# Performance work log

Measured on AMD Instinct MI355X. Metric: run time of the kernel, lower is better.

## Reference

```python
import jax, jax.numpy as jnp
import numpy as np

B, T, C, H = 4, 2048, 768, 12
D = C // H  # head dim = 64
EPS = 1e-5


def setup_inputs() -> dict:
    key = jax.random.key(0)
    ks = jax.random.split(key, 12)
    s = lambda fan_in: 1.0 / np.sqrt(fan_in)
    return {
        "x": jax.random.normal(ks[0], (B, T, C), dtype=jnp.float32),
        "ln1_g": jnp.ones((C,), jnp.float32),
        "ln1_b": jnp.zeros((C,), jnp.float32),
        "w_attn": jax.random.normal(ks[1], (C, 3 * C), jnp.float32) * s(C),
        "b_attn": jnp.zeros((3 * C,), jnp.float32),
        "w_aproj": jax.random.normal(ks[2], (C, C), jnp.float32) * s(C),
        "b_aproj": jnp.zeros((C,), jnp.float32),
        "ln2_g": jnp.ones((C,), jnp.float32),
        "ln2_b": jnp.zeros((C,), jnp.float32),
        "w_fc": jax.random.normal(ks[3], (C, 4 * C), jnp.float32) * s(C),
        "b_fc": jnp.zeros((4 * C,), jnp.float32),
        "w_mproj": jax.random.normal(ks[4], (4 * C, C), jnp.float32) * s(4 * C),
        "b_mproj": jnp.zeros((C,), jnp.float32),
    }


def _layernorm(x, g, b):
    mu = jnp.mean(x, axis=-1, keepdims=True)
    var = jnp.mean(jnp.square(x - mu), axis=-1, keepdims=True)
    return (x - mu) * jax.lax.rsqrt(var + EPS) * g + b


def _attention(h, w_attn, b_attn, w_aproj, b_aproj):
    qkv = h @ w_attn + b_attn                          # [B,T,3C]
    q, k, v = jnp.split(qkv, 3, axis=-1)
    q = q.reshape(B, T, H, D)
    k = k.reshape(B, T, H, D)
    v = v.reshape(B, T, H, D)
    att = jnp.einsum("bqhd,bkhd->bhqk", q, k) * (1.0 / np.sqrt(D))
    causal = jnp.tril(jnp.ones((T, T), bool))
    att = jnp.where(causal, att, -jnp.inf)
    att = jax.nn.softmax(att, axis=-1)
    y = jnp.einsum("bhqk,bkhd->bqhd", att, v).reshape(B, T, C)
    return y @ w_aproj + b_aproj


def reference(x, ln1_g, ln1_b, w_attn, b_attn, w_aproj, b_aproj,
              ln2_g, ln2_b, w_fc, b_fc, w_mproj, b_mproj):
    x = x + _attention(_layernorm(x, ln1_g, ln1_b), w_attn, b_attn, w_aproj, b_aproj)
    h = _layernorm(x, ln2_g, ln2_b)
    h = jax.nn.gelu(h @ w_fc + b_fc, approximate=True)  # tanh approximation, matches F.gelu(approximate='tanh')
    x = x + (h @ w_mproj + b_mproj)
    return x
```

## Files before the change

kernel.cpp:

```cpp
#include <hip/hip_runtime.h>


typedef unsigned short ushortT;
typedef unsigned int uintT;
typedef __attribute__((ext_vector_type(8))) __bf16 bf16x8;
typedef __attribute__((ext_vector_type(4))) float f32x4;

#define MFMA16(a, b, c) __builtin_amdgcn_mfma_f32_16x16x32_bf16(a, b, c, 0, 0, 0)

__device__ inline float b2f(ushortT u) {
  return __uint_as_float(((uintT)u) << 16);
}
__device__ inline ushortT f2b(float f) {
  uintT x = __float_as_uint(f);
  uintT r = x + 0x7fffu + ((x >> 16) & 1u);
  return (ushortT)(r >> 16);
}
__device__ inline uintT pack_bf2(float a, float b) {
  return __builtin_amdgcn_perm(__float_as_uint(b), __float_as_uint(a),
                               0x07060302u);
}

__device__ inline float fast_exp2(float x) {
#if __has_builtin(__builtin_amdgcn_exp2f)
  return __builtin_amdgcn_exp2f(x);
#else
  return exp2f(x);
#endif
}

__device__ inline float gelu_tanh(float v) {
  float t = 0.7978845608028654f * (v + 0.044715f * v * v * v);
  return v / (1.0f + __expf(-2.0f * t));
}

__device__ __forceinline__ void glds16(const ushortT* g, ushortT* l) {
  __builtin_amdgcn_global_load_lds(
      (const __attribute__((address_space(1))) unsigned int*)(const void*)g,
      (__attribute__((address_space(3))) unsigned int*)(void*)l, 16, 0, 0);
}

__global__ __launch_bounds__(256) void detect_dtype(
    const ushortT* __restrict__ w, int* __restrict__ flag) {
  __shared__ int red;
  if (threadIdx.x == 0) red = 0;
  __syncthreads();
  int crazy = 0;
  for (int i = threadIdx.x; i < 4096; i += 256) {
    uintT e = (w[2 * i] >> 7) & 0xFF;
    if (e >= 150) crazy = 1;
  }
  if (crazy) atomicOr(&red, 1);
  __syncthreads();
  if (threadIdx.x == 0) *flag = red;
}

struct VecArgs {
  const void* src[8];
  int n[8];
  int dstoff[8];
};
__global__ __launch_bounds__(256) void convert_vecs(
    VecArgs a, ushortT* __restrict__ pv, const int* __restrict__ flag) {
  int fl = *flag;
  int t = blockIdx.y;
  int i = blockIdx.x * 256 + threadIdx.x;
  if (i >= a.n[t]) return;
  float v = fl ? ((const float*)a.src[t])[i] : b2f(((const ushortT*)a.src[t])[i]);
  pv[a.dstoff[t] + i] = f2b(v);
}

__global__ __launch_bounds__(256) void transpose_any(
    const void* __restrict__ in, ushortT* __restrict__ out, int K, int N,
    const int* __restrict__ flag) {
  __shared__ ushortT t[32][33];
  int fl = *flag;
  int n0 = blockIdx.x * 32, k0 = blockIdx.y * 32;
  int x = threadIdx.x, y0 = threadIdx.y;
#pragma unroll
  for (int i = y0; i < 32; i += 8) {
    size_t idx = (size_t)(k0 + i) * N + n0 + x;
    t[i][x] = fl ? f2b(((const float*)in)[idx]) : ((const ushortT*)in)[idx];
  }
  __syncthreads();
#pragma unroll
  for (int i = y0; i < 32; i += 8)
    out[(size_t)(n0 + i) * K + k0 + x] = t[x][i];
}

__global__ __launch_bounds__(256) void vtrans_kernel(
    const ushortT* __restrict__ qkv, ushortT* __restrict__ vt) {
  const int T = 2048, C3 = 2304;
  __shared__ ushortT tile[64][65];
  int bh = blockIdx.y;
  int b = bh / 12, h = bh % 12;
  int t0 = blockIdx.x * 64;
  int col = threadIdx.x & 63, rowi = threadIdx.x >> 6;
#pragma unroll
  for (int rr = rowi; rr < 64; rr += 4)
    tile[rr][col] =
        qkv[((size_t)(b * T + t0 + rr)) * C3 + 1536 + h * 64 + col];
  __syncthreads();
#pragma unroll
  for (int dd = rowi; dd < 64; dd += 4)
    vt[((size_t)bh * 64 + dd) * T + t0 + col] = tile[col][dd];
}

template <int MODE>
__global__ __launch_bounds__(256) void ln_kernel(
    const void* __restrict__ xin, const ushortT* __restrict__ g,
    const ushortT* __restrict__ bb, ushortT* __restrict__ out,
    const int* __restrict__ flag) {
  const int C = 768;
  bool f32;
  if constexpr (MODE == 1) f32 = true; else f32 = (*flag != 0);
  size_t base = (size_t)blockIdx.x * C;
  int tid = threadIdx.x;
  const float* xf = (const float*)xin;
  const ushortT* xb = (const ushortT*)xin;
  float v0 = f32 ? xf[base + tid]       : b2f(xb[base + tid]);
  float v1 = f32 ? xf[base + tid + 256] : b2f(xb[base + tid + 256]);
  float v2 = f32 ? xf[base + tid + 512] : b2f(xb[base + tid + 512]);
  float s = v0 + v1 + v2;
  float q = v0 * v0 + v1 * v1 + v2 * v2;
#pragma unroll
  for (int off = 32; off; off >>= 1) {
    s += __shfl_xor(s, off);
    q += __shfl_xor(q, off);
  }
  __shared__ float as_[4], aq_[4];
  if ((tid & 63) == 0) { as_[tid >> 6] = s; aq_[tid >> 6] = q; }
  __syncthreads();
  s = as_[0] + as_[1] + as_[2] + as_[3];
  q = aq_[0] + aq_[1] + aq_[2] + aq_[3];
  float mu = s * (1.0f / 768.0f);
  float var = q * (1.0f / 768.0f) - mu * mu;
  float rs = rsqrtf(var + 1e-5f);
  ushortT* orow = out + base;
  orow[tid]       = f2b((v0 - mu) * rs * b2f(g[tid])       + b2f(bb[tid]));
  orow[tid + 256] = f2b((v1 - mu) * rs * b2f(g[tid + 256]) + b2f(bb[tid + 256]));
  orow[tid + 512] = f2b((v2 - mu) * rs * b2f(g[tid + 512]) + b2f(bb[tid + 512]));
}

template <int EPI, int BN>
__global__ __launch_bounds__(256, 2) void gemm_8p(
    const ushortT* __restrict__ A, const ushortT* __restrict__ Bt,
    const ushortT* __restrict__ bias, const void* __restrict__ res,
    void* __restrict__ out, int N, int K, int lda, int nbm, int nbn,
    const int* __restrict__ flag) {
  constexpr int MI = (BN == 256) ? 8 : 4;
  constexpr int NI = 4;
  __shared__ ushortT As3[3][128 * 32];
  __shared__ ushortT Bs3[3][BN * 32];
  int fl = (EPI == 2) ? *flag : 0;
  int tid = threadIdx.x;
  int lane = tid & 63, wave = tid >> 6;
  int quad = lane >> 4, n = lane & 15;
  int wm, wn;
  if constexpr (BN == 256) { wm = 0; wn = wave * 64; }
  else { wm = (wave >> 1) * 64; wn = (wave & 1) * 64; }
  int l = blockIdx.x;
  int xcd = l & 7, j = l >> 3;
  int per = (nbm >> 3) * nbn;
  int js = j % per, sp = j / per;
  int m0 = (xcd * (nbm >> 3) + js / nbn) * 128;
  int n0 = (js % nbn) * BN;
  int koff = sp * K;

  int trow = tid >> 2;
  int tc = (((tid & 3) ^ ((trow >> 1) & 3)) << 3);
  const ushortT* ga = A + (size_t)(m0 + trow) * lda + koff + tc;
  const ushortT* gb = Bt + (size_t)(n0 + trow) * lda + koff + tc;

  const int cs = (quad ^ ((n >> 1) & 3)) << 3;

  int kt = K >> 5;
  f32x4 acc[MI][NI] = {};

  auto stage = [&](int tt, int slot) {
    int k0 = tt << 5;
    ushortT* la = &As3[slot][0] + wave * 512;
    ushortT* lb = &Bs3[slot][0] + wave * 512;
    glds16(ga + k0, la);
    glds16(ga + (size_t)64 * lda + k0, la + 2048);
    glds16(gb + k0, lb);
    glds16(gb + (size_t)64 * lda + k0, lb + 2048);
    if constexpr (BN == 256) {
      glds16(gb + (size_t)128 * lda + k0, lb + 4096);
      glds16(gb + (size_t)192 * lda + k0, lb + 6144);
    }
  };

  stage(0, 0);
  stage(1, 1);
  if constexpr (BN == 256)
    asm volatile("s_waitcnt vmcnt(6)" ::: "memory");
  else
    asm volatile("s_waitcnt vmcnt(4)" ::: "memory");
  __builtin_amdgcn_s_barrier();

  int cur = 0;
  for (int t = 0; t < kt; ++t) {
    const ushortT* ca = &As3[cur][0];
    const ushortT* cb = &Bs3[cur][0];
    int nxt = cur + 2; if (nxt >= 3) nxt -= 3;
    bool pf = (t + 2) < kt;
    int pk0 = (t + 2) << 5;
    ushortT* la = &As3[nxt][0] + wave * 512;
    ushortT* lb = &Bs3[nxt][0] + wave * 512;

    bf16x8 af[4], bfr[NI];
#pragma unroll
    for (int i = 0; i < 4; ++i)
      af[i] = *(const bf16x8*)(ca + (wm + i * 16 + n) * 32 + cs);
#pragma unroll
    for (int i = 0; i < NI; ++i)
      bfr[i] = *(const bf16x8*)(cb + (wn + i * 16 + n) * 32 + cs);
    if (pf) {
      glds16(ga + pk0, la);
      glds16(ga + (size_t)64 * lda + pk0, la + 2048);
      glds16(gb + pk0, lb);
      if constexpr (BN == 128)
        glds16(gb + (size_t)64 * lda + pk0, lb + 2048);
    }
    __builtin_amdgcn_s_barrier();
    __builtin_amdgcn_s_setprio(1);
#pragma unroll
    for (int mi = 0; mi < 4; ++mi)
#pragma unroll
      for (int ni = 0; ni < NI; ++ni)
        acc[mi][ni] = MFMA16(af[mi], bfr[ni], acc[mi][ni]);
    __builtin_amdgcn_s_setprio(0);
    if constexpr (BN == 256) {
      __builtin_amdgcn_s_barrier();
#pragma unroll
      for (int i = 0; i < 4; ++i)
        af[i] = *(const bf16x8*)(ca + (64 + i * 16 + n) * 32 + cs);
      if (pf) {
        glds16(gb + (size_t)64 * lda + pk0, lb + 2048);
        glds16(gb + (size_t)128 * lda + pk0, lb + 4096);
        glds16(gb + (size_t)192 * lda + pk0, lb + 6144);
      }
      __builtin_amdgcn_s_barrier();
      __builtin_amdgcn_s_setprio(1);
#pragma unroll
      for (int mi = 0; mi < 4; ++mi)
#pragma unroll
        for (int ni = 0; ni < NI; ++ni)
          acc[4 + mi][ni] = MFMA16(af[mi], bfr[ni], acc[4 + mi][ni]);
      __builtin_amdgcn_s_setprio(0);
    }
    if (pf) {
      if constexpr (BN == 256)
        asm volatile("s_waitcnt vmcnt(6)" ::: "memory");
      else
        asm volatile("s_waitcnt vmcnt(4)" ::: "memory");
    } else {
      asm volatile("s_waitcnt vmcnt(0)" ::: "memory");
    }
    __builtin_amdgcn_s_barrier();

    cur = cur + 1; if (cur == 3) cur = 0;
  }

  float* po = nullptr;
  if constexpr (EPI == 4) po = sp ? (float*)res : (float*)out;
#pragma unroll
  for (int mi = 0; mi < MI; ++mi) {
#pragma unroll
    for (int ni = 0; ni < NI; ++ni) {
      int gc = n0 + wn + ni * 16 + n;
      float bv = (EPI == 4) ? 0.0f : b2f(bias[gc]);
      int gr0 = m0 + wm + mi * 16 + quad * 4;
#pragma unroll
      for (int r = 0; r < 4; ++r) {
        size_t idx = (size_t)(gr0 + r) * N + gc;
        float v = acc[mi][ni][r] + bv;
        if constexpr (EPI == 1) {
          v = gelu_tanh(v);
          ((ushortT*)out)[idx] = f2b(v);
        } else if constexpr (EPI == 2) {
          v += fl ? ((const float*)res)[idx] : b2f(((const ushortT*)res)[idx]);
          ((float*)out)[idx] = v;
        } else if constexpr (EPI == 3) {
          v += ((const float*)res)[idx];
          if (fl) ((float*)out)[idx] = v;
          else    ((ushortT*)out)[idx] = f2b(v);
        } else if constexpr (EPI == 4) {
          po[idx] = v;
        } else {
          ((ushortT*)out)[idx] = f2b(v);
        }
      }
    }
  }
}

__global__ __launch_bounds__(256) void mproj_reduce(
    const float* __restrict__ P0, const float* __restrict__ P1,
    const float* __restrict__ res, const ushortT* __restrict__ bias,
    void* __restrict__ out, const int* __restrict__ flag) {
  int fl = *flag;
  size_t i0 = ((size_t)blockIdx.x * 256 + threadIdx.x) * 8;
  int col = (int)(i0 % 768);
  float o[8];
#pragma unroll
  for (int j = 0; j < 8; j += 4) {
    float4 a = *(const float4*)(P0 + i0 + j);
    float4 b = *(const float4*)(P1 + i0 + j);
    float4 r = *(const float4*)(res + i0 + j);
    o[j + 0] = a.x + b.x + r.x + b2f(bias[col + j + 0]);
    o[j + 1] = a.y + b.y + r.y + b2f(bias[col + j + 1]);
    o[j + 2] = a.z + b.z + r.z + b2f(bias[col + j + 2]);
    o[j + 3] = a.w + b.w + r.w + b2f(bias[col + j + 3]);
  }
  if (fl) {
    float* of = (float*)out;
#pragma unroll
    for (int j = 0; j < 8; ++j) of[i0 + j] = o[j];
  } else {
    uint4 pk;
    pk.x = pack_bf2(o[0], o[1]);
    pk.y = pack_bf2(o[2], o[3]);
    pk.z = pack_bf2(o[4], o[5]);
    pk.w = pack_bf2(o[6], o[7]);
    *(uint4*)((ushortT*)out + i0) = pk;
  }
}

__global__ __launch_bounds__(256) void attn_kernel(
    const ushortT* __restrict__ qkv, const ushortT* __restrict__ vt,
    ushortT* __restrict__ y) {
  const int T = 2048, C3 = 2304;
  constexpr int LDP = 72;
  __shared__ ushortT Ks[2][64 * 64];
  __shared__ ushortT Vs[2][64 * 64];
  __shared__ ushortT Ps[4 * 16 * LDP];
  int bh = blockIdx.y;
  int b = bh / 12, h = bh % 12;
  int pj = blockIdx.x;
  int tid = threadIdx.x;
  int lane = tid & 63, wave = tid >> 6;
  int quad = lane >> 4, n = lane & 15, n7 = n & 7;

  const ushortT* base = qkv + (size_t)b * T * C3;
  const ushortT* kbase = base + 768 + h * 64;
  const ushortT* vbase = vt + (size_t)bh * 64 * T;
  ushortT* myP = Ps + wave * 16 * LDP;

  const float QS = 0.18033688011112042f;
  const float MB = 20.0f;

  int qtA = pj, qtB = 31 - pj;
  int nA = qtA + 1, ntot = 33;

  int srow = lane >> 3, scol = lane & 7;
  const ushortT* kg =
      kbase + (size_t)(wave * 16 + srow) * C3 + ((scol ^ srow) << 3);
  const ushortT* vg =
      vbase + (size_t)(wave * 16 + srow) * T + ((scol ^ srow) << 3);

  const int c0 = (quad ^ n7) << 3;
  const int c1 = ((4 + quad) ^ n7) << 3;

  int qt = qtA;
  int qw = qt * 64 + wave * 16;
  bf16x8 aq[2];
  {
    const ushortT* qrow = base + (size_t)(qw + n) * C3 + h * 64 + quad * 8;
#pragma unroll
    for (int dh = 0; dh < 2; ++dh) {
      union { ushortT u[8]; bf16x8 v; } tmp;
#pragma unroll
      for (int j = 0; j < 8; ++j) tmp.u[j] = f2b(b2f(qrow[dh * 32 + j]) * QS);
      aq[dh] = tmp.v;
    }
  }
  f32x4 Ot[4] = {};
  float l_ = 0.f;

  auto stage = [&](int kt_, int buf) {
    int kof = kt_ << 6;
    ushortT* lk = &Ks[buf][0] + wave * 1024;
    ushortT* lv = &Vs[buf][0] + wave * 1024;
    glds16(kg + (size_t)kof * C3, lk);
    glds16(kg + (size_t)(kof + 8) * C3, lk + 512);
    glds16(vg + kof, lv);
    glds16(vg + (size_t)8 * T + kof, lv + 512);
  };

  stage(0, 0);
  __syncthreads();

  int cur = 0;
  for (int t = 0; t < ntot; ++t) {
    int kt = (t < nA) ? t : t - nA;
    if (t + 1 < ntot) {
      int ktn = (t + 1 < nA) ? t + 1 : t + 1 - nA;
      stage(ktn, cur ^ 1);
    }
    const ushortT* ks = &Ks[cur][0];
    const ushortT* vs = &Vs[cur][0];

    f32x4 St[4];
#pragma unroll
    for (int g = 0; g < 4; ++g) {
      bf16x8 ka0 = *(const bf16x8*)(ks + (g * 16 + n) * 64 + c0);
      bf16x8 ka1 = *(const bf16x8*)(ks + (g * 16 + n) * 64 + c1);
      f32x4 z = {};
      z = MFMA16(ka0, aq[0], z);
      St[g] = MFMA16(ka1, aq[1], z);
    }
    if (kt == qt) {
      int lim = wave * 16 + n;
#pragma unroll
      for (int g = 0; g < 4; ++g)
#pragma unroll
        for (int r = 0; r < 4; ++r)
          if (g * 16 + quad * 4 + r > lim) St[g][r] = -1e30f;
    }
    float ls = 0.f;
#pragma unroll
    for (int g = 0; g < 4; ++g) {
      float p0 = fast_exp2(St[g][0] - MB);
      float p1 = fast_exp2(St[g][1] - MB);
      float p2 = fast_exp2(St[g][2] - MB);
      float p3 = fast_exp2(St[g][3] - MB);
      ls += (p0 + p1) + (p2 + p3);
      uint2 pk;
      pk.x = pack_bf2(p0, p1);
      pk.y = pack_bf2(p2, p3);
      *(uint2*)(myP + n * LDP + g * 16 + quad * 4) = pk;
    }
    ls += __shfl_xor(ls, 16);
    ls += __shfl_xor(ls, 32);
    l_ += ls;

    bf16x8 pb0 = *(const bf16x8*)(myP + n * LDP + quad * 8);
    bf16x8 pb1 = *(const bf16x8*)(myP + n * LDP + 32 + quad * 8);
#pragma unroll
    for (int dt = 0; dt < 4; ++dt) {
      bf16x8 va0 = *(const bf16x8*)(vs + (dt * 16 + n) * 64 + c0);
      bf16x8 va1 = *(const bf16x8*)(vs + (dt * 16 + n) * 64 + c1);
      Ot[dt] = MFMA16(va0, pb0, Ot[dt]);
      Ot[dt] = MFMA16(va1, pb1, Ot[dt]);
    }

    if (kt == qt) {
      float inv = 1.0f / l_;
      int qg = qw + n;
#pragma unroll
      for (int dt = 0; dt < 4; ++dt) {
        uint2 o;
        o.x = pack_bf2(Ot[dt][0] * inv, Ot[dt][1] * inv);
        o.y = pack_bf2(Ot[dt][2] * inv, Ot[dt][3] * inv);
        *(uint2*)(y + (size_t)(b * T + qg) * 768 + h * 64 + dt * 16 +
                  quad * 4) = o;
      }
      if (t + 1 < ntot) {
        qt = qtB;
        qw = qt * 64 + wave * 16;
        const ushortT* qrow =
            base + (size_t)(qw + n) * C3 + h * 64 + quad * 8;
#pragma unroll
        for (int dh = 0; dh < 2; ++dh) {
          union { ushortT u[8]; bf16x8 v; } tmp;
#pragma unroll
          for (int j = 0; j < 8; ++j)
            tmp.u[j] = f2b(b2f(qrow[dh * 32 + j]) * QS);
          aq[dh] = tmp.v;
        }
#pragma unroll
        for (int dt = 0; dt < 4; ++dt)
#pragma unroll
          for (int r = 0; r < 4; ++r) Ot[dt][r] = 0.f;
        l_ = 0.f;
      }
    }
    __syncthreads();
    cur ^= 1;
  }
}

extern "C" void kernel_launch(void* const* d_in, const int* in_sizes, int n_in,
                              void* d_out, int out_size, void* d_ws,
                              size_t ws_size, hipStream_t stream) {
  (void)in_sizes; (void)n_in; (void)out_size; (void)ws_size;
  const void* x       = d_in[0];
  const void* w_attn  = d_in[3];
  const void* w_aproj = d_in[5];
  const void* w_fc    = d_in[9];
  const void* w_mproj = d_in[11];

  char* ws = (char*)d_ws;
  ushortT* h1  = (ushortT*)(ws);
  ushortT* qkv = (ushortT*)(ws + 12582912);
  ushortT* yb  = (ushortT*)(ws + 50331648);
  float*   x1  = (float*)(ws + 62914560);
  ushortT* fcg = (ushortT*)(ws + 88080384);
  ushortT* wT0 = (ushortT*)(ws + 138412032);
  ushortT* wT1 = (ushortT*)(ws + 141950976);
  ushortT* wT2 = (ushortT*)(ws + 143130624);
  ushortT* wT3 = (ushortT*)(ws + 147849216);
  ushortT* pv  = (ushortT*)(ws + 152567808);
  int*     flag = (int*)(ws + 152600576);
  ushortT* vt  = h1;
  ushortT* h2  = yb;
  float*   P0  = (float*)(ws);
  float*   P1  = (float*)(ws + 25165824);

  const int O_LN1G = 0, O_LN1B = 768, O_BATT = 1536, O_BAPR = 3840,
            O_LN2G = 4608, O_LN2B = 5376, O_BFC = 6144, O_BMPR = 9216;

  detect_dtype<<<1, 256, 0, stream>>>((const ushortT*)w_fc, flag);

  VecArgs va;
  va.src[0] = d_in[1];  va.n[0] = 768;  va.dstoff[0] = O_LN1G;
  va.src[1] = d_in[2];  va.n[1] = 768;  va.dstoff[1] = O_LN1B;
  va.src[2] = d_in[4];  va.n[2] = 2304; va.dstoff[2] = O_BATT;
  va.src[3] = d_in[6];  va.n[3] = 768;  va.dstoff[3] = O_BAPR;
  va.src[4] = d_in[7];  va.n[4] = 768;  va.dstoff[4] = O_LN2G;
  va.src[5] = d_in[8];  va.n[5] = 768;  va.dstoff[5] = O_LN2B;
  va.src[6] = d_in[10]; va.n[6] = 3072; va.dstoff[6] = O_BFC;
  va.src[7] = d_in[12]; va.n[7] = 768;  va.dstoff[7] = O_BMPR;
  convert_vecs<<<dim3(12, 8), 256, 0, stream>>>(va, pv, flag);

  dim3 tb(32, 8);
  transpose_any<<<dim3(72, 24), tb, 0, stream>>>(w_attn, wT0, 768, 2304, flag);
  transpose_any<<<dim3(24, 24), tb, 0, stream>>>(w_aproj, wT1, 768, 768, flag);
  transpose_any<<<dim3(96, 24), tb, 0, stream>>>(w_fc, wT2, 768, 3072, flag);
  transpose_any<<<dim3(24, 96), tb, 0, stream>>>(w_mproj, wT3, 3072, 768, flag);

  ln_kernel<0><<<8192, 256, 0, stream>>>(x, pv + O_LN1G, pv + O_LN1B, h1, flag);
  gemm_8p<0, 256><<<576, 256, 0, stream>>>(
      h1, wT0, pv + O_BATT, nullptr, qkv, 2304, 768, 768, 64, 9, flag);
  vtrans_kernel<<<dim3(32, 48), 256, 0, stream>>>(qkv, vt);
  attn_kernel<<<dim3(16, 48), 256, 0, stream>>>(qkv, vt, yb);
  gemm_8p<2, 128><<<384, 256, 0, stream>>>(
      yb, wT1, pv + O_BAPR, x, x1, 768, 768, 768, 64, 6, flag);
  ln_kernel<1><<<8192, 256, 0, stream>>>(x1, pv + O_LN2G, pv + O_LN2B, h2, flag);
  gemm_8p<1, 256><<<768, 256, 0, stream>>>(
      h2, wT2, pv + O_BFC, nullptr, fcg, 3072, 768, 768, 64, 12, flag);
  gemm_8p<4, 128><<<768, 256, 0, stream>>>(
      fcg, wT3, nullptr, P1, P0, 768, 1536, 3072, 64, 6, flag);
  mproj_reduce<<<3072, 256, 0, stream>>>(
      P0, P1, x1, pv + O_BMPR, d_out, flag);
}
```

Measured before the change: 419.7 us.

## Merge weight prep kernels into one launch and drop mproj split-K reduce

Fuses dtype detection, bias/gain conversion and the four weight transposes into a single prep_kernel launch, with each block computing the dtype flag from a sparse sample via ballot. It also replaces the two-way split-K mproj GEMM plus separate reduce kernel with a single full-K GEMM using the fused residual+bias epilogue (EPI 3). This removes several launches and the fp32 partial-sum round trip through memory. In exchange the mproj GEMM runs 384 blocks with K=3072, which lowers parallelism on a large GPU. The dtype check now samples fewer elements.

```diff
diff --git a/kernel.cpp b/kernel.cpp
--- a/kernel.cpp
+++ b/kernel.cpp
@@ -40,52 +40,75 @@
       (__attribute__((address_space(3))) unsigned int*)(void*)l, 16, 0, 0);
 }
 
-__global__ __launch_bounds__(256) void detect_dtype(
-    const ushortT* __restrict__ w, int* __restrict__ flag) {
-  __shared__ int red;
-  if (threadIdx.x == 0) red = 0;
-  __syncthreads();
-  int crazy = 0;
-  for (int i = threadIdx.x; i < 4096; i += 256) {
-    uintT e = (w[2 * i] >> 7) & 0xFF;
-    if (e >= 150) crazy = 1;
-  }
-  if (crazy) atomicOr(&red, 1);
-  __syncthreads();
-  if (threadIdx.x == 0) *flag = red;
-}
-
 struct VecArgs {
   const void* src[8];
   int n[8];
   int dstoff[8];
 };
-__global__ __launch_bounds__(256) void convert_vecs(
-    VecArgs a, ushortT* __restrict__ pv, const int* __restrict__ flag) {
-  int fl = *flag;
-  int t = blockIdx.y;
-  int i = blockIdx.x * 256 + threadIdx.x;
-  if (i >= a.n[t]) return;
-  float v = fl ? ((const float*)a.src[t])[i] : b2f(((const ushortT*)a.src[t])[i]);
-  pv[a.dstoff[t] + i] = f2b(v);
-}
-
-__global__ __launch_bounds__(256) void transpose_any(
-    const void* __restrict__ in, ushortT* __restrict__ out, int K, int N,
-    const int* __restrict__ flag) {
-  __shared__ ushortT t[32][33];
-  int fl = *flag;
-  int n0 = blockIdx.x * 32, k0 = blockIdx.y * 32;
-  int x = threadIdx.x, y0 = threadIdx.y;
+
+__global__ __launch_bounds__(256) void prep_kernel(
+    const void* __restrict__ w_attn, const void* __restrict__ w_aproj,
+    const void* __restrict__ w_fc, const void* __restrict__ w_mproj,
+    VecArgs va, ushortT* __restrict__ wT0, ushortT* __restrict__ wT1,
+    ushortT* __restrict__ wT2, ushortT* __restrict__ wT3,
+    ushortT* __restrict__ pv, int* __restrict__ flag) {
+  __shared__ int sfl;
+  __shared__ ushortT tile[32][33];
+  int tid = threadIdx.x;
+  {
+    int crazy = 0;
+    if (tid < 64) {
+      uintT e = (((const ushortT*)w_fc)[2 * (tid * 64)] >> 7) & 0xFF;
+      crazy = (e >= 150) ? 1 : 0;
+    }
+    unsigned long long m = __ballot(crazy != 0);
+    if (tid == 0) sfl = (m != 0ull) ? 1 : 0;
+    __syncthreads();
+  }
+  int fl = sfl;
+  int b = (int)blockIdx.x;
+  if (b == 0 && tid == 0) *flag = fl;
+
+  const int T0 = 1728;
+  const int T1 = T0 + 576;
+  const int T2 = T1 + 2304;
+  const int T3 = T2 + 2304;
+
+  const void* in = nullptr;
+  ushortT* out = nullptr;
+  int K = 0, N = 0, gx = 0, t = 0;
+  if (b < T0)      { in = w_attn;  out = wT0; K = 768;  N = 2304; gx = 72; t = b; }
+  else if (b < T1) { in = w_aproj; out = wT1; K = 768;  N = 768;  gx = 24; t = b - T0; }
+  else if (b < T2) { in = w_fc;    out = wT2; K = 768;  N = 3072; gx = 96; t = b - T1; }
+  else if (b < T3) { in = w_mproj; out = wT3; K = 3072; N = 768;  gx = 24; t = b - T2; }
+  else {
+    int c = b - T3;
+    int v = 0;
+    for (;;) {
+      int nch = (va.n[v] + 255) >> 8;
+      if (c < nch) break;
+      c -= nch; ++v;
+    }
+    int i = c * 256 + tid;
+    if (i < va.n[v]) {
+      float x = fl ? ((const float*)va.src[v])[i]
+                   : b2f(((const ushortT*)va.src[v])[i]);
+      pv[va.dstoff[v] + i] = f2b(x);
+    }
+    return;
+  }
+
+  int n0 = (t % gx) * 32, k0 = (t / gx) * 32;
+  int x = tid & 31, y0 = tid >> 5;
 #pragma unroll
   for (int i = y0; i < 32; i += 8) {
     size_t idx = (size_t)(k0 + i) * N + n0 + x;
-    t[i][x] = fl ? f2b(((const float*)in)[idx]) : ((const ushortT*)in)[idx];
+    tile[i][x] = fl ? f2b(((const float*)in)[idx]) : ((const ushortT*)in)[idx];
   }
   __syncthreads();
 #pragma unroll
   for (int i = y0; i < 32; i += 8)
-    out[(size_t)(n0 + i) * K + k0 + x] = t[x][i];
+    out[(size_t)(n0 + i) * K + k0 + x] = tile[x][i];
 }
 
 __global__ __launch_bounds__(256) void vtrans_kernel(
@@ -152,7 +175,7 @@
   constexpr int NI = 4;
   __shared__ ushortT As3[3][128 * 32];
   __shared__ ushortT Bs3[3][BN * 32];
-  int fl = (EPI == 2) ? *flag : 0;
+  int fl = (EPI >= 2) ? *flag : 0;
   int tid = threadIdx.x;
   int lane = tid & 63, wave = tid >> 6;
   int quad = lane >> 4, n = lane & 15;
@@ -296,38 +319,6 @@
   }
 }
 
-__global__ __launch_bounds__(256) void mproj_reduce(
-    const float* __restrict__ P0, const float* __restrict__ P1,
-    const float* __restrict__ res, const ushortT* __restrict__ bias,
-    void* __restrict__ out, const int* __restrict__ flag) {
-  int fl = *flag;
-  size_t i0 = ((size_t)blockIdx.x * 256 + threadIdx.x) * 8;
-  int col = (int)(i0 % 768);
-  float o[8];
-#pragma unroll
-  for (int j = 0; j < 8; j += 4) {
-    float4 a = *(const float4*)(P0 + i0 + j);
-    float4 b = *(const float4*)(P1 + i0 + j);
-    float4 r = *(const float4*)(res + i0 + j);
-    o[j + 0] = a.x + b.x + r.x + b2f(bias[col + j + 0]);
-    o[j + 1] = a.y + b.y + r.y + b2f(bias[col + j + 1]);
-    o[j + 2] = a.z + b.z + r.z + b2f(bias[col + j + 2]);
-    o[j + 3] = a.w + b.w + r.w + b2f(bias[col + j + 3]);
-  }
-  if (fl) {
-    float* of = (float*)out;
-#pragma unroll
-    for (int j = 0; j < 8; ++j) of[i0 + j] = o[j];
-  } else {
-    uint4 pk;
-    pk.x = pack_bf2(o[0], o[1]);
-    pk.y = pack_bf2(o[2], o[3]);
-    pk.z = pack_bf2(o[4], o[5]);
-    pk.w = pack_bf2(o[6], o[7]);
-    *(uint4*)((ushortT*)out + i0) = pk;
-  }
-}
-
 __global__ __launch_bounds__(256) void attn_kernel(
     const ushortT* __restrict__ qkv, const ushortT* __restrict__ vt,
     ushortT* __restrict__ y) {
@@ -506,13 +497,9 @@
   int*     flag = (int*)(ws + 152600576);
   ushortT* vt  = h1;
   ushortT* h2  = yb;
-  float*   P0  = (float*)(ws);
-  float*   P1  = (float*)(ws + 25165824);
 
   const int O_LN1G = 0, O_LN1B = 768, O_BATT = 1536, O_BAPR = 3840,
             O_LN2G = 4608, O_LN2B = 5376, O_BFC = 6144, O_BMPR = 9216;
-
-  detect_dtype<<<1, 256, 0, stream>>>((const ushortT*)w_fc, flag);
 
   VecArgs va;
   va.src[0] = d_in[1];  va.n[0] = 768;  va.dstoff[0] = O_LN1G;
@@ -523,13 +510,9 @@
   va.src[5] = d_in[8];  va.n[5] = 768;  va.dstoff[5] = O_LN2B;
   va.src[6] = d_in[10]; va.n[6] = 3072; va.dstoff[6] = O_BFC;
   va.src[7] = d_in[12]; va.n[7] = 768;  va.dstoff[7] = O_BMPR;
-  convert_vecs<<<dim3(12, 8), 256, 0, stream>>>(va, pv, flag);
-
-  dim3 tb(32, 8);
-  transpose_any<<<dim3(72, 24), tb, 0, stream>>>(w_attn, wT0, 768, 2304, flag);
-  transpose_any<<<dim3(24, 24), tb, 0, stream>>>(w_aproj, wT1, 768, 768, flag);
-  transpose_any<<<dim3(96, 24), tb, 0, stream>>>(w_fc, wT2, 768, 3072, flag);
-  transpose_any<<<dim3(24, 96), tb, 0, stream>>>(w_mproj, wT3, 3072, 768, flag);
+
+  prep_kernel<<<6951, 256, 0, stream>>>(
+      w_attn, w_aproj, w_fc, w_mproj, va, wT0, wT1, wT2, wT3, pv, flag);
 
   ln_kernel<0><<<8192, 256, 0, stream>>>(x, pv + O_LN1G, pv + O_LN1B, h1, flag);
   gemm_8p<0, 256><<<576, 256, 0, stream>>>(
@@ -541,8 +524,6 @@
   ln_kernel<1><<<8192, 256, 0, stream>>>(x1, pv + O_LN2G, pv + O_LN2B, h2, flag);
   gemm_8p<1, 256><<<768, 256, 0, stream>>>(
       h2, wT2, pv + O_BFC, nullptr, fcg, 3072, 768, 768, 64, 12, flag);
-  gemm_8p<4, 128><<<768, 256, 0, stream>>>(
-      fcg, wT3, nullptr, P1, P0, 768, 1536, 3072, 64, 6, flag);
-  mproj_reduce<<<3072, 256, 0, stream>>>(
-      P0, P1, x1, pv + O_BMPR, d_out, flag);
-}
+  gemm_8p<3, 128><<<384, 256, 0, stream>>>(
+      fcg, wT3, pv + O_BMPR, x1, d_out, 768, 3072, 3072, 64, 6, flag);
+}
```

After: 409.1 us. 2.5% less time.
